# Optimization experiments

Measured on AMD Instinct MI355X. Metric: run time of the kernel, lower is better.

Reference implementation:

```python
import jax, jax.numpy as jnp
import numpy as np

B, L = 8, 2048          # images, lines per image
C_IN, HW = 256, 128     # backbone feature channels, spatial size
DIM_LOI = 128
N_PTS0, N_PTS1 = 32, 8  # sampled points per line, after maxpool
SCALE = N_PTS0 // N_PTS1
EPS = 1e-5


def setup_inputs() -> dict:
    key = jax.random.key(0)
    ks = jax.random.split(key, 24)
    d = {}
    d['feature'] = jax.random.normal(ks[0], (B, C_IN, HW, HW), jnp.float32)
    # line endpoints in pixel coords [0, 128)
    d['lines'] = jax.random.uniform(ks[1], (B, L, 2, 2), jnp.float32) * HW
    # fc1: 1x1 conv 256 -> 128
    d['fc1_w'] = jax.random.normal(ks[2], (DIM_LOI, C_IN), jnp.float32) * 0.05
    d['fc1_b'] = jnp.zeros((DIM_LOI,), jnp.float32)
    planes = DIM_LOI // 2
    def bn(k, c):
        k1, k2, k3 = jax.random.split(k, 3)
        return (jax.random.normal(k1, (c,), jnp.float32) * 0.1 + 1.0,
                jax.random.normal(k2, (c,), jnp.float32) * 0.1,
                jax.random.normal(k3, (c,), jnp.float32) * 0.05,
                jax.random.uniform(jax.random.fold_in(k, 7), (c,), jnp.float32, 0.5, 1.5))
    d['bn1_g'], d['bn1_b'], d['bn1_m'], d['bn1_v'] = bn(ks[3], DIM_LOI)
    d['conv1_w'] = jax.random.normal(ks[4], (planes, DIM_LOI), jnp.float32) * 0.05
    d['conv1_b'] = jnp.zeros((planes,), jnp.float32)
    d['bn2_g'], d['bn2_b'], d['bn2_m'], d['bn2_v'] = bn(ks[5], planes)
    d['conv2_w'] = jax.random.normal(ks[6], (planes, planes, 3), jnp.float32) * 0.05
    d['conv2_b'] = jnp.zeros((planes,), jnp.float32)
    d['bn3_g'], d['bn3_b'], d['bn3_m'], d['bn3_v'] = bn(ks[7], planes)
    d['conv3_w'] = jax.random.normal(ks[8], (DIM_LOI, planes), jnp.float32) * 0.05
    d['conv3_b'] = jnp.zeros((DIM_LOI,), jnp.float32)
    d['fc2_w'] = jax.random.normal(ks[9], (1, DIM_LOI * N_PTS1), jnp.float32) * 0.02
    d['fc2_b'] = jnp.zeros((1,), jnp.float32)
    return d


def _bn(x, g, b, m, v):
    # x: [N, C, T], eval-mode batchnorm
    s = g * jax.lax.rsqrt(v + EPS)
    return x * s[None, :, None] + (b - m * s)[None, :, None]


def _loi_forward(feature, lines, fc1_w, fc1_b,
                 bn1_g, bn1_b, bn1_m, bn1_v, conv1_w, conv1_b,
                 bn2_g, bn2_b, bn2_m, bn2_v, conv2_w, conv2_b,
                 bn3_g, bn3_b, bn3_m, bn3_v, conv3_w, conv3_b,
                 fc2_w, fc2_b):
    # fc1: 1x1 conv -> [B, DIM_LOI, H, W]
    x = jnp.einsum('oc,bchw->bohw', fc1_w, feature) + fc1_b[None, :, None, None]

    # sample N_PTS0 points per line: p = p0*lam + p1*(1-lam) - 0.5
    lam = jnp.linspace(0.0, 1.0, N_PTS0, dtype=lines.dtype)  # [P]
    pts = (lines[:, :, 0, None, :] * lam[None, None, :, None]
           + lines[:, :, 1, None, :] * (1.0 - lam[None, None, :, None]) - 0.5)  # [B,L,P,2]
    px, py = pts[..., 0], pts[..., 1]
    px0 = jnp.clip(jnp.floor(px), 0.0, HW - 1.0)
    py0 = jnp.clip(jnp.floor(py), 0.0, HW - 1.0)
    px1 = jnp.clip(px0 + 1.0, 0.0, HW - 1.0)
    py1 = jnp.clip(py0 + 1.0, 0.0, HW - 1.0)
    px0l, py0l = px0.astype(jnp.int32), py0.astype(jnp.int32)
    px1l, py1l = px1.astype(jnp.int32), py1.astype(jnp.int32)

    def gather(f, ix, iy):  # f: [C,H,W], ix/iy: [L,P] -> [C,L,P]
        return f[:, ix, iy]

    gat = jax.vmap(gather)  # over batch
    xp = (gat(x, px0l, py0l) * ((px1 - px) * (py1 - py))[:, None]
          + gat(x, px1l, py0l) * ((px - px0) * (py1 - py))[:, None]
          + gat(x, px0l, py1l) * ((px1 - px) * (py - py0))[:, None]
          + gat(x, px1l, py1l) * ((px - px0) * (py - py0))[:, None])  # [B,C,L,P]

    xp = xp.transpose(0, 2, 1, 3).reshape(B * L, DIM_LOI, N_PTS0)  # [N,C,P]
    # MaxPool1d(kernel=stride=SCALE)
    xp = xp.reshape(B * L, DIM_LOI, N_PTS1, SCALE).max(axis=-1)  # [N,C,T=8]

    # Bottleneck1D residual: x + op(x)
    h = jax.nn.relu(_bn(xp, bn1_g, bn1_b, bn1_m, bn1_v))
    h = jnp.einsum('oc,nct->not', conv1_w, h) + conv1_b[None, :, None]
    h = jax.nn.relu(_bn(h, bn2_g, bn2_b, bn2_m, bn2_v))
    h = jax.lax.conv_general_dilated(h, conv2_w, (1,), [(1, 1)],
                                     dimension_numbers=('NCH', 'OIH', 'NCH'))
    h = h + conv2_b[None, :, None]
    h = jax.nn.relu(_bn(h, bn3_g, bn3_b, bn3_m, bn3_v))
    h = jnp.einsum('oc,nct->not', conv3_w, h) + conv3_b[None, :, None]
    xp = xp + h

    # fc2: ReLU -> Linear(dim_loi*n_pts1, 1)
    flat = jax.nn.relu(xp).reshape(B * L, DIM_LOI * N_PTS1)
    logits = (flat @ fc2_w.T + fc2_b).reshape(-1)  # [B*L]
    return logits


def reference(feature, lines, fc1_w, fc1_b,
              bn1_g, bn1_b, bn1_m, bn1_v, conv1_w, conv1_b,
              bn2_g, bn2_b, bn2_m, bn2_v, conv2_w, conv2_b,
              bn3_g, bn3_b, bn3_m, bn3_v, conv3_w, conv3_b,
              fc2_w, fc2_b):
    return _loi_forward(feature, lines, fc1_w, fc1_b,
                        bn1_g, bn1_b, bn1_m, bn1_v, conv1_w, conv1_b,
                        bn2_g, bn2_b, bn2_m, bn2_v, conv2_w, conv2_b,
                        bn3_g, bn3_b, bn3_m, bn3_v, conv3_w, conv3_b,
                        fc2_w, fc2_b)
```

## Files before the change

### kernel.cpp

```cpp
#include <hip/hip_runtime.h>

#define EPSBN 1e-5f

typedef _Float16 f16;
typedef _Float16 f16x8 __attribute__((ext_vector_type(8)));
typedef _Float16 f16x4 __attribute__((ext_vector_type(4)));
typedef _Float16 f16x2 __attribute__((ext_vector_type(2)));
typedef float    f32x4 __attribute__((ext_vector_type(4)));

#define AS1 __attribute__((address_space(1)))
#define AS3 __attribute__((address_space(3)))

__device__ inline f16x8 hmax8(f16x8 a, f16x8 b) {
    f16x8 r;
    #pragma unroll
    for (int i = 0; i < 8; ++i) r[i] = a[i] > b[i] ? a[i] : b[i];
    return r;
}
__device__ inline f16x8 relu8(f16x8 v) {
    f16x8 r;
    #pragma unroll
    for (int i = 0; i < 8; ++i) r[i] = v[i] > (f16)0.f ? v[i] : (f16)0.f;
    return r;
}

__global__ void wprep_kernel(const float* __restrict__ fc1w,
                             const float* __restrict__ w1,
                             const float* __restrict__ w2,
                             const float* __restrict__ w3,
                             f16* __restrict__ dst) {
    const int i = blockIdx.x * 256 + threadIdx.x;
    float v;
    if (i < 32768) {
        const int k8   = i & 7;
        const int lane = (i >> 3) & 63;
        const int t    = (i >> 9) & 3;
        const int ow   = (i >> 11) & 1;
        const int s    = (i >> 12) & 7;
        const int n16l = lane & 15, quadl = lane >> 4;
        v = fc1w[(ow * 64 + t * 16 + n16l) * 256 + s * 32 + quadl * 8 + k8];
    }
    else if (i < 40960) v = w1[i - 32768];
    else if (i < 53248) {
        const int j = i - 40960, tau = j >> 12, rest = j & 4095;
        v = w2[rest * 3 + tau];
    } else              v = w3[i - 53248];
    dst[i] = (f16)v;
}

__global__ __launch_bounds__(1024, 4)
void fc1_mfma(const float* __restrict__ feat,
              const f16*   __restrict__ wfrag,
              const float* __restrict__ bias,
              f16*         __restrict__ xmap) {
    __shared__ f16 wlds[32768];
    __shared__ union {
        f16 xb[2][256][32];
        f16 epi[64][136];
    } u;

    const int tid  = threadIdx.x;
    const int wv   = tid >> 6;
    const int lane = tid & 63;
    const int n16  = lane & 15, quad = lane >> 4;
    const int pw   = wv >> 1;
    const int ow   = wv & 1;
    const int img  = blockIdx.x & 7;
    const int p0   = (blockIdx.x >> 3) << 8;

    const float* fimg = feat + (((size_t)img) << 22);

    const int spt = tid & 255, chgrp = tid >> 8;
    const float* sbase = fimg + (((size_t)(chgrp * 8)) << 14) + p0 + spt;
    const int swcol = (chgrp ^ ((spt >> 1) & 3)) << 3;

    f32x4 acc[2][4];
    #pragma unroll
    for (int ptg = 0; ptg < 2; ++ptg)
        #pragma unroll
        for (int t = 0; t < 4; ++t) acc[ptg][t] = (f32x4){0.f, 0.f, 0.f, 0.f};

    #pragma unroll
    for (int c4 = 0; c4 < 4; ++c4) {
        const int c = wv + 16 * c4;
        __builtin_amdgcn_global_load_lds((const AS1 void*)(wfrag + c * 512 + lane * 8),
                                         (AS3 void*)(wlds + c * 512), 16, 0, 0);
    }
    float st[2][8];
    #pragma unroll
    for (int c = 0; c < 8; ++c) {
        st[0][c] = sbase[(size_t)c << 14];
        st[1][c] = sbase[524288 + ((size_t)c << 14)];
    }
    {
        f16x8 h;
        #pragma unroll
        for (int c = 0; c < 8; ++c) h[c] = (f16)st[0][c];
        *(f16x8*)&u.xb[0][spt][swcol] = h;
    }
    asm volatile("s_waitcnt vmcnt(0)" ::: "memory");
    __syncthreads();

    #pragma unroll
    for (int s = 0; s < 8; ++s) {
        if (s < 6) {
            #pragma unroll
            for (int c = 0; c < 8; ++c)
                st[s & 1][c] = sbase[(size_t)(s + 2) * 524288 + ((size_t)c << 14)];
        }

        f16x8 wf[4];
        #pragma unroll
        for (int t = 0; t < 4; ++t)
            wf[t] = *(const f16x8*)&wlds[((((s * 2 + ow) * 4 + t) * 64) + lane) * 8];

        f16x8 xf[2];
        #pragma unroll
        for (int ptg = 0; ptg < 2; ++ptg) {
            const int pt = pw * 32 + ptg * 16 + n16;
            xf[ptg] = *(const f16x8*)&u.xb[s & 1][pt][(quad ^ ((pt >> 1) & 3)) << 3];
        }

        #pragma unroll
        for (int ptg = 0; ptg < 2; ++ptg)
            #pragma unroll
            for (int t = 0; t < 4; ++t)
                acc[ptg][t] = __builtin_amdgcn_mfma_f32_16x16x32_f16(wf[t], xf[ptg],
                                                                     acc[ptg][t], 0, 0, 0);

        if (s < 7) {
            f16x8 h;
            #pragma unroll
            for (int c = 0; c < 8; ++c) h[c] = (f16)st[(s + 1) & 1][c];
            *(f16x8*)&u.xb[(s + 1) & 1][spt][swcol] = h;

            __builtin_amdgcn_sched_barrier(0);
            asm volatile("s_waitcnt lgkmcnt(0)" ::: "memory");
            __builtin_amdgcn_sched_barrier(0);
            __builtin_amdgcn_s_barrier();
            __builtin_amdgcn_sched_barrier(0);
        }
    }

    #pragma unroll
    for (int P = 0; P < 4; ++P) {
        __syncthreads();
        if ((pw >> 1) == P) {
            #pragma unroll
            for (int ptg = 0; ptg < 2; ++ptg) {
                const int rowl = (pw & 1) * 32 + ptg * 16 + n16;
                #pragma unroll
                for (int t = 0; t < 4; ++t) {
                    const int o = ow * 64 + t * 16 + quad * 4;
                    const float4 bq = *(const float4*)&bias[o];
                    f16x4 hv;
                    hv[0] = (f16)(acc[ptg][t][0] + bq.x);
                    hv[1] = (f16)(acc[ptg][t][1] + bq.y);
                    hv[2] = (f16)(acc[ptg][t][2] + bq.z);
                    hv[3] = (f16)(acc[ptg][t][3] + bq.w);
                    *(f16x4*)&u.epi[rowl][o] = hv;
                }
            }
        }
        __syncthreads();
        {
            const int rowl = tid >> 4, seg = tid & 15;
            const float4 v = *(const float4*)&u.epi[rowl][seg * 8];
            *(float4*)&xmap[(((size_t)(img * 16384 + p0 + P * 64 + rowl)) << 7) + seg * 8] = v;
        }
    }
}

__global__ __launch_bounds__(256)
void loi_kernel(const f16*   __restrict__ x,
                const float* __restrict__ lines,
                const f16*   __restrict__ wsp,
                const float* __restrict__ bn1g, const float* __restrict__ bn1b,
                const float* __restrict__ bn1m, const float* __restrict__ bn1v,
                const float* __restrict__ b1,
                const float* __restrict__ bn2g, const float* __restrict__ bn2b,
                const float* __restrict__ bn2m, const float* __restrict__ bn2v,
                const float* __restrict__ b2,
                const float* __restrict__ bn3g, const float* __restrict__ bn3b,
                const float* __restrict__ bn3m, const float* __restrict__ bn3v,
                const float* __restrict__ b3,
                const float* __restrict__ fc2w, const float* __restrict__ fc2b,
                float* __restrict__ out) {
    __shared__ f16 xp[64][136];
    __shared__ alignas(16) union {
        struct { int toff[256][4]; f16 twgt[256][4]; } tp;
        struct { f16 h1[80][72]; f16 h2[64][72]; } cv;
    } u;
    __shared__ f16 s1h[128], t1h[128];
    __shared__ float s2f[64], t2f[64], s3f[64], t3f[64], b1f[64], b2f[64];
    __shared__ float b3f[128];
    __shared__ float wsum[4][8];

    const f16* w1f16 = wsp + 32768;
    const f16* w2f16 = wsp + 40960;
    const f16* w3f16 = wsp + 53248;

    const int tid  = threadIdx.x;
    const int wv   = tid >> 6, lane = tid & 63;
    const int n16  = lane & 15, quad = lane >> 4;
    const int img  = blockIdx.x & 7;
    const int mblk = blockIdx.x >> 3;

    if (tid < 128) {
        const float s = bn1g[tid] * rsqrtf(bn1v[tid] + EPSBN);
        s1h[tid] = (f16)s; t1h[tid] = (f16)(bn1b[tid] - bn1m[tid] * s);
    }
    if (tid < 64) {
        const float s = bn2g[tid] * rsqrtf(bn2v[tid] + EPSBN);
        s2f[tid] = s; t2f[tid] = bn2b[tid] - bn2m[tid] * s;
        b1f[tid] = b1[tid];
    } else if (tid < 128) {
        const int c = tid - 64;
        const float s = bn3g[c] * rsqrtf(bn3v[c] + EPSBN);
        s3f[c] = s; t3f[c] = bn3b[c] - bn3m[c] * s;
        b2f[c] = b2[c];
    } else {
        b3f[tid - 128] = b3[tid - 128];
    }

    {
        const int li = tid >> 5, pt = tid & 31;
        const int gl = img * 2048 + mblk * 8 + li;
        const float4 ln = *(const float4*)&lines[gl * 4];
        const float lam = (float)pt * (1.0f / 31.0f);
        const float px = ln.x * lam + ln.z * (1.f - lam) - 0.5f;
        const float py = ln.y * lam + ln.w * (1.f - lam) - 0.5f;
        const float px0 = fminf(fmaxf(floorf(px), 0.f), 127.f);
        const float py0 = fminf(fmaxf(floorf(py), 0.f), 127.f);
        const float px1 = fminf(px0 + 1.f, 127.f);
        const float py1 = fminf(py0 + 1.f, 127.f);
        const int ix0 = (int)px0, iy0 = (int)py0;
        const int ix1 = (int)px1, iy1 = (int)py1;
        u.tp.toff[tid][0] = (((ix0 << 7) + iy0) << 7);
        u.tp.toff[tid][1] = (((ix1 << 7) + iy0) << 7);
        u.tp.toff[tid][2] = (((ix0 << 7) + iy1) << 7);
        u.tp.toff[tid][3] = (((ix1 << 7) + iy1) << 7);
        const float wx1 = px1 - px, wx0 = px - px0;
        const float wy1 = py1 - py, wy0 = py - py0;
        u.tp.twgt[tid][0] = (f16)(wx1 * wy1); u.tp.twgt[tid][1] = (f16)(wx0 * wy1);
        u.tp.twgt[tid][2] = (f16)(wx1 * wy0); u.tp.twgt[tid][3] = (f16)(wx0 * wy0);
    }
    __syncthreads();

    {
        const int h  = lane >> 5;
        const int sh = (lane >> 4) & 1;
        const int j  = lane & 15;
        const int li = wv * 2 + h;
        const f16* xbh = x + (((size_t)img) << 21) + 8 * j;
        #pragma unroll
        for (int t = 0; t < 8; ++t) {
            f16x8 m;
            #pragma unroll
            for (int q = 0; q < 8; ++q) m[q] = (f16)(-60000.f);
            #pragma unroll
            for (int ss = 0; ss < 2; ++ss) {
                const int combo = li * 32 + t * 4 + sh * 2 + ss;
                const int4  off = *(const int4*)&u.tp.toff[combo][0];
                const f16x4 tw  = *(const f16x4*)&u.tp.twgt[combo][0];
                const f16x8 g00 = *(const f16x8*)(xbh + off.x);
                const f16x8 g10 = *(const f16x8*)(xbh + off.y);
                const f16x8 g01 = *(const f16x8*)(xbh + off.z);
                const f16x8 g11 = *(const f16x8*)(xbh + off.w);
                f16x8 w0, w1v, w2v, w3v;
                #pragma unroll
                for (int q = 0; q < 8; ++q) {
                    w0[q] = tw[0]; w1v[q] = tw[1]; w2v[q] = tw[2]; w3v[q] = tw[3];
                }
                const f16x8 v = g00 * w0 + g10 * w1v + g01 * w2v + g11 * w3v;
                m = hmax8(m, v);
            }
            union { f16x8 v8; int i4[4]; } cv;
            cv.v8 = m;
            #pragma unroll
            for (int q = 0; q < 4; ++q) cv.i4[q] = __shfl_xor(cv.i4[q], 16, 64);
            m = hmax8(m, cv.v8);
            if (sh == 0) *(f16x8*)&xp[li * 8 + t][8 * j] = m;
        }
    }
    __syncthreads();

    {
        const int r = tid >> 4, seg = tid & 15;
        const int row = (r >> 1) * 10 + (r & 1) * 9;
        *(unsigned long long*)&u.cv.h1[row][seg * 4] = 0ull;
    }

    {
        const int o_lane = wv * 16 + n16;
        f32x4 acc1[4];
        #pragma unroll
        for (int nt = 0; nt < 4; ++nt) acc1[nt] = (f32x4){0.f, 0.f, 0.f, 0.f};
        #pragma unroll
        for (int ks = 0; ks < 4; ++ks) {
            const int k = ks * 32 + quad * 8;
            const f16x8 a  = *(const f16x8*)&w1f16[o_lane * 128 + k];
            const f16x8 s8 = *(const f16x8*)&s1h[k];
            const f16x8 t8 = *(const f16x8*)&t1h[k];
            #pragma unroll
            for (int nt = 0; nt < 4; ++nt) {
                const f16x8 raw = *(const f16x8*)&xp[nt * 16 + n16][k];
                const f16x8 bf = relu8(raw * s8 + t8);
                acc1[nt] = __builtin_amdgcn_mfma_f32_16x16x32_f16(a, bf, acc1[nt], 0, 0, 0);
            }
        }
        #pragma unroll
        for (int nt = 0; nt < 4; ++nt) {
            const int n = nt * 16 + n16;
            const int nprow = (n >> 3) * 10 + (n & 7) + 1;
            #pragma unroll
            for (int r = 0; r < 4; ++r) {
                const int o = wv * 16 + quad * 4 + r;
                const float v = fmaxf((acc1[nt][r] + b1f[o]) * s2f[o] + t2f[o], 0.f);
                u.cv.h1[nprow][o] = (f16)v;
            }
        }
    }
    __syncthreads();

    {
        const int o_lane = wv * 16 + n16;
        f32x4 acc2[4];
        #pragma unroll
        for (int nt = 0; nt < 4; ++nt) acc2[nt] = (f32x4){0.f, 0.f, 0.f, 0.f};
        #pragma unroll
        for (int d = 0; d < 3; ++d) {
            const f16* A2 = w2f16 + d * 4096;
            #pragma unroll
            for (int ks = 0; ks < 2; ++ks) {
                const int k = ks * 32 + quad * 8;
                const f16x8 a = *(const f16x8*)&A2[o_lane * 64 + k];
                #pragma unroll
                for (int nt = 0; nt < 4; ++nt) {
                    const int n = nt * 16 + n16;
                    const int row = (n >> 3) * 10 + (n & 7) + d;
                    const f16x8 bf = *(const f16x8*)&u.cv.h1[row][k];
                    acc2[nt] = __builtin_amdgcn_mfma_f32_16x16x32_f16(a, bf, acc2[nt], 0, 0, 0);
                }
            }
        }
        #pragma unroll
        for (int nt = 0; nt < 4; ++nt) {
            const int n = nt * 16 + n16;
            #pragma unroll
            for (int r = 0; r < 4; ++r) {
                const int o = wv * 16 + quad * 4 + r;
                const float v = fmaxf((acc2[nt][r] + b2f[o]) * s3f[o] + t3f[o], 0.f);
                u.cv.h2[n][o] = (f16)v;
            }
        }
    }
    __syncthreads();

    {
        const int col = n16 & 7, obase = wv * 16 + quad * 4;
        float fcv[2][4];
        #pragma unroll
        for (int h = 0; h < 2; ++h)
            #pragma unroll
            for (int r = 0; r < 4; ++r)
                fcv[h][r] = fc2w[(h * 64 + obase + r) * 8 + col];

        f32x4 acc3[2][4];
        #pragma unroll
        for (int h = 0; h < 2; ++h)
            #pragma unroll
            for (int nt = 0; nt < 4; ++nt) acc3[h][nt] = (f32x4){0.f, 0.f, 0.f, 0.f};
        #pragma unroll
        for (int ks = 0; ks < 2; ++ks) {
            const int k = ks * 32 + quad * 8;
            const f16x8 a0 = *(const f16x8*)&w3f16[(wv * 16 + n16) * 64 + k];
            const f16x8 a1 = *(const f16x8*)&w3f16[(64 + wv * 16 + n16) * 64 + k];
            #pragma unroll
            for (int nt = 0; nt < 4; ++nt) {
                const f16x8 bf = *(const f16x8*)&u.cv.h2[nt * 16 + n16][k];
                acc3[0][nt] = __builtin_amdgcn_mfma_f32_16x16x32_f16(a0, bf, acc3[0][nt], 0, 0, 0);
                acc3[1][nt] = __builtin_amdgcn_mfma_f32_16x16x32_f16(a1, bf, acc3[1][nt], 0, 0, 0);
            }
        }
        float part[4] = {0.f, 0.f, 0.f, 0.f};
        #pragma unroll
        for (int h = 0; h < 2; ++h) {
            const float4 bq = *(const float4*)&b3f[h * 64 + obase];
            const float bqa[4] = {bq.x, bq.y, bq.z, bq.w};
            #pragma unroll
            for (int nt = 0; nt < 4; ++nt) {
                const int n = nt * 16 + n16;
                const f16x4 rx = *(const f16x4*)&xp[n][h * 64 + obase];
                float p = 0.f;
                #pragma unroll
                for (int r = 0; r < 4; ++r) {
                    float v = acc3[h][nt][r] + bqa[r] + (float)rx[r];
                    v = fmaxf(v, 0.f);
                    p += v * fcv[h][r];
                }
                part[nt] += p;
            }
        }
        #pragma unroll
        for (int off_i = 0; off_i < 5; ++off_i) {
            const int off = (int[]){1, 2, 4, 16, 32}[off_i];
            part[0] += __shfl_xor(part[0], off, 64);
            part[1] += __shfl_xor(part[1], off, 64);
            part[2] += __shfl_xor(part[2], off, 64);
            part[3] += __shfl_xor(part[3], off, 64);
        }
        if ((lane & 55) == 0) {
            const int par = (lane >> 3) & 1;
            wsum[wv][0 + par] = part[0];
            wsum[wv][2 + par] = part[1];
            wsum[wv][4 + par] = part[2];
            wsum[wv][6 + par] = part[3];
        }
    }
    __syncthreads();

    if (tid < 8) {
        const float s = wsum[0][tid] + wsum[1][tid] + wsum[2][tid] + wsum[3][tid];
        out[img * 2048 + mblk * 8 + tid] = s + fc2b[0];
    }
}

extern "C" void kernel_launch(void* const* d_in, const int* in_sizes, int n_in,
                              void* d_out, int out_size, void* d_ws, size_t ws_size,
                              hipStream_t stream) {
    const float* feature = (const float*)d_in[0];
    const float* lines   = (const float*)d_in[1];
    const float* fc1_w   = (const float*)d_in[2];
    const float* fc1_b   = (const float*)d_in[3];
    const float* bn1g    = (const float*)d_in[4];
    const float* bn1b    = (const float*)d_in[5];
    const float* bn1m    = (const float*)d_in[6];
    const float* bn1v    = (const float*)d_in[7];
    const float* w1      = (const float*)d_in[8];
    const float* b1      = (const float*)d_in[9];
    const float* bn2g    = (const float*)d_in[10];
    const float* bn2b    = (const float*)d_in[11];
    const float* bn2m    = (const float*)d_in[12];
    const float* bn2v    = (const float*)d_in[13];
    const float* w2      = (const float*)d_in[14];
    const float* b2      = (const float*)d_in[15];
    const float* bn3g    = (const float*)d_in[16];
    const float* bn3b    = (const float*)d_in[17];
    const float* bn3m    = (const float*)d_in[18];
    const float* bn3v    = (const float*)d_in[19];
    const float* w3      = (const float*)d_in[20];
    const float* b3      = (const float*)d_in[21];
    const float* fc2w    = (const float*)d_in[22];
    const float* fc2b    = (const float*)d_in[23];

    f16* xmap = (f16*)d_ws;
    f16* wsp  = (f16*)((char*)d_ws + (size_t)32 * 1024 * 1024);

    wprep_kernel<<<240, 256, 0, stream>>>(fc1_w, w1, w2, w3, wsp);
    fc1_mfma<<<512, 1024, 0, stream>>>(feature, wsp, fc1_b, xmap);
    loi_kernel<<<2048, 256, 0, stream>>>(xmap, lines, wsp,
                                         bn1g, bn1b, bn1m, bn1v, b1,
                                         bn2g, bn2b, bn2m, bn2v, b2,
                                         bn3g, bn3b, bn3m, bn3v, b3,
                                         fc2w, fc2b, (float*)d_out);
}
```

Measured before the change: 278.1 us.

## Double fc1 pixel tile per block and load features as float4

The fc1 MFMA kernel now processes 512 pixels per block instead of 256, halving the grid to 256 blocks. Each wave computes two pixel tiles, which amortises the per-block weight load into LDS over twice the work. Feature staging switches from scalar loads to float4 loads with a new LDS swizzle. The cost is a larger LDS footprint, more accumulator registers and fewer blocks to spread across CUs.

```diff
diff --git a/kernel.cpp b/kernel.cpp
--- a/kernel.cpp
+++ b/kernel.cpp
@@ -55,30 +55,50 @@
               f16*         __restrict__ xmap) {
     __shared__ f16 wlds[32768];
     __shared__ union {
-        f16 xb[2][256][32];
-        f16 epi[64][136];
+        f16 xb[2][512][32];
+        f16 epi[128][136];
     } u;
 
     const int tid  = threadIdx.x;
     const int wv   = tid >> 6;
     const int lane = tid & 63;
     const int n16  = lane & 15, quad = lane >> 4;
-    const int pw   = wv >> 1;
     const int ow   = wv & 1;
+    const int tw0  = wv >> 1;
     const int img  = blockIdx.x & 7;
-    const int p0   = (blockIdx.x >> 3) << 8;
+    const int p0   = (blockIdx.x >> 3) << 9;
 
     const float* fimg = feat + (((size_t)img) << 22);
 
-    const int spt = tid & 255, chgrp = tid >> 8;
-    const float* sbase = fimg + (((size_t)(chgrp * 8)) << 14) + p0 + spt;
-    const int swcol = (chgrp ^ ((spt >> 1) & 3)) << 3;
-
-    f32x4 acc[2][4];
-    #pragma unroll
-    for (int ptg = 0; ptg < 2; ++ptg)
-        #pragma unroll
-        for (int t = 0; t < 4; ++t) acc[ptg][t] = (f32x4){0.f, 0.f, 0.f, 0.f};
+    const int chg = tid >> 7;
+    const int pg  = tid & 127;
+    const float* sb = fimg + p0 + pg * 4;
+
+    f32x4 acc[2][2][4];
+    #pragma unroll
+    for (int h = 0; h < 2; ++h)
+        #pragma unroll
+        for (int ptg = 0; ptg < 2; ++ptg)
+            #pragma unroll
+            for (int t = 0; t < 4; ++t) acc[h][ptg][t] = (f32x4){0.f, 0.f, 0.f, 0.f};
+
+    float4 st4[4];
+    auto load_stage = [&](int s) {
+        #pragma unroll
+        for (int cc = 0; cc < 4; ++cc)
+            st4[cc] = *(const float4*)(sb + (((size_t)(s * 32 + chg * 4 + cc)) << 14));
+    };
+    auto write_stage = [&](int s) {
+        #pragma unroll
+        for (int pp = 0; pp < 4; ++pp) {
+            const int pt   = pg * 4 + pp;
+            const int slot = (chg >> 1) ^ ((pt >> 2) & 3);
+            f16x4 h;
+            h[0] = (f16)st4[0][pp]; h[1] = (f16)st4[1][pp];
+            h[2] = (f16)st4[2][pp]; h[3] = (f16)st4[3][pp];
+            *(f16x4*)&u.xb[s & 1][pt][slot * 8 + (chg & 1) * 4] = h;
+        }
+    };
 
     #pragma unroll
     for (int c4 = 0; c4 < 4; ++c4) {
@@ -86,53 +106,39 @@
         __builtin_amdgcn_global_load_lds((const AS1 void*)(wfrag + c * 512 + lane * 8),
                                          (AS3 void*)(wlds + c * 512), 16, 0, 0);
     }
-    float st[2][8];
-    #pragma unroll
-    for (int c = 0; c < 8; ++c) {
-        st[0][c] = sbase[(size_t)c << 14];
-        st[1][c] = sbase[524288 + ((size_t)c << 14)];
-    }
-    {
-        f16x8 h;
-        #pragma unroll
-        for (int c = 0; c < 8; ++c) h[c] = (f16)st[0][c];
-        *(f16x8*)&u.xb[0][spt][swcol] = h;
-    }
+    load_stage(0);
+    write_stage(0);
     asm volatile("s_waitcnt vmcnt(0)" ::: "memory");
     __syncthreads();
 
     #pragma unroll
     for (int s = 0; s < 8; ++s) {
-        if (s < 6) {
-            #pragma unroll
-            for (int c = 0; c < 8; ++c)
-                st[s & 1][c] = sbase[(size_t)(s + 2) * 524288 + ((size_t)c << 14)];
-        }
+        if (s < 7) load_stage(s + 1);
 
         f16x8 wf[4];
         #pragma unroll
         for (int t = 0; t < 4; ++t)
-            wf[t] = *(const f16x8*)&wlds[((((s * 2 + ow) * 4 + t) * 64) + lane) * 8];
-
-        f16x8 xf[2];
-        #pragma unroll
-        for (int ptg = 0; ptg < 2; ++ptg) {
-            const int pt = pw * 32 + ptg * 16 + n16;
-            xf[ptg] = *(const f16x8*)&u.xb[s & 1][pt][(quad ^ ((pt >> 1) & 3)) << 3];
-        }
-
-        #pragma unroll
-        for (int ptg = 0; ptg < 2; ++ptg)
-            #pragma unroll
-            for (int t = 0; t < 4; ++t)
-                acc[ptg][t] = __builtin_amdgcn_mfma_f32_16x16x32_f16(wf[t], xf[ptg],
-                                                                     acc[ptg][t], 0, 0, 0);
+            wf[t] = *(const f16x8*)&wlds[(((s * 2 + ow) * 4 + t) * 64 + lane) * 8];
+
+        #pragma unroll
+        for (int h = 0; h < 2; ++h) {
+            const int tile = tw0 + h * 8;
+            f16x8 xf[2];
+            #pragma unroll
+            for (int ptg = 0; ptg < 2; ++ptg) {
+                const int pt = tile * 32 + ptg * 16 + n16;
+                xf[ptg] = *(const f16x8*)&u.xb[s & 1][pt][(quad ^ ((pt >> 2) & 3)) << 3];
+            }
+            #pragma unroll
+            for (int ptg = 0; ptg < 2; ++ptg)
+                #pragma unroll
+                for (int t = 0; t < 4; ++t)
+                    acc[h][ptg][t] = __builtin_amdgcn_mfma_f32_16x16x32_f16(
+                        wf[t], xf[ptg], acc[h][ptg][t], 0, 0, 0);
+        }
 
         if (s < 7) {
-            f16x8 h;
-            #pragma unroll
-            for (int c = 0; c < 8; ++c) h[c] = (f16)st[(s + 1) & 1][c];
-            *(f16x8*)&u.xb[(s + 1) & 1][spt][swcol] = h;
+            write_stage(s + 1);
 
             __builtin_amdgcn_sched_barrier(0);
             asm volatile("s_waitcnt lgkmcnt(0)" ::: "memory");
@@ -145,28 +151,31 @@
     #pragma unroll
     for (int P = 0; P < 4; ++P) {
         __syncthreads();
-        if ((pw >> 1) == P) {
+        const int hh = (P >= 2);
+        if ((wv >> 3) == (P & 1)) {
             #pragma unroll
             for (int ptg = 0; ptg < 2; ++ptg) {
-                const int rowl = (pw & 1) * 32 + ptg * 16 + n16;
+                const int rowl = (tw0 & 3) * 32 + ptg * 16 + n16;
                 #pragma unroll
                 for (int t = 0; t < 4; ++t) {
                     const int o = ow * 64 + t * 16 + quad * 4;
                     const float4 bq = *(const float4*)&bias[o];
                     f16x4 hv;
-                    hv[0] = (f16)(acc[ptg][t][0] + bq.x);
-                    hv[1] = (f16)(acc[ptg][t][1] + bq.y);
-                    hv[2] = (f16)(acc[ptg][t][2] + bq.z);
-                    hv[3] = (f16)(acc[ptg][t][3] + bq.w);
+                    hv[0] = (f16)(acc[hh][ptg][t][0] + bq.x);
+                    hv[1] = (f16)(acc[hh][ptg][t][1] + bq.y);
+                    hv[2] = (f16)(acc[hh][ptg][t][2] + bq.z);
+                    hv[3] = (f16)(acc[hh][ptg][t][3] + bq.w);
                     *(f16x4*)&u.epi[rowl][o] = hv;
                 }
             }
         }
         __syncthreads();
-        {
-            const int rowl = tid >> 4, seg = tid & 15;
+        #pragma unroll
+        for (int it = 0; it < 2; ++it) {
+            const int idx = it * 1024 + tid;
+            const int rowl = idx >> 4, seg = idx & 15;
             const float4 v = *(const float4*)&u.epi[rowl][seg * 8];
-            *(float4*)&xmap[(((size_t)(img * 16384 + p0 + P * 64 + rowl)) << 7) + seg * 8] = v;
+            *(float4*)&xmap[(((size_t)(img * 16384 + p0 + P * 128 + rowl)) << 7) + seg * 8] = v;
         }
     }
 }
@@ -458,7 +467,7 @@
     f16* wsp  = (f16*)((char*)d_ws + (size_t)32 * 1024 * 1024);
 
     wprep_kernel<<<240, 256, 0, stream>>>(fc1_w, w1, w2, w3, wsp);
-    fc1_mfma<<<512, 1024, 0, stream>>>(feature, wsp, fc1_b, xmap);
+    fc1_mfma<<<256, 1024, 0, stream>>>(feature, wsp, fc1_b, xmap);
     loi_kernel<<<2048, 256, 0, stream>>>(xmap, lines, wsp,
                                          bn1g, bn1b, bn1m, bn1v, b1,
                                          bn2g, bn2b, bn2m, bn2v, b2,
```

New measurement: 277.3 us. No clear change (-0.3%).
